# Kernel tuning notes

Measured on AMD Instinct MI355X. Metric: run time of the kernel, lower is better.

The kernel has to match this reference:

```python
import jax, jax.numpy as jnp
import numpy as np

DELAY = 4
SKIP = 2
NF = 8
HS = 256
EPS = 1e-5


def setup_inputs() -> dict:
    key = jax.random.key(0)
    ks = jax.random.split(key, 11)
    B, NP, NO, T = 16, 512, 512, 2048
    predictor = jax.random.normal(ks[0], (B, NP, T), dtype=jnp.float32)
    to_order = jax.random.normal(ks[1], (B, NO, T), dtype=jnp.float32)
    trilinear = jax.random.normal(ks[2], (NF, NO, NP), dtype=jnp.float32) / np.float32(np.sqrt(NP * NO))
    w_o = jax.random.normal(ks[3], (HS, NO), dtype=jnp.float32) / np.float32(np.sqrt(NO))
    b_o = jax.random.normal(ks[4], (HS,), dtype=jnp.float32) * 0.01
    w_p = jax.random.normal(ks[5], (HS, NP), dtype=jnp.float32) / np.float32(np.sqrt(NP))
    b_p = jax.random.normal(ks[6], (HS,), dtype=jnp.float32) * 0.01
    bn_gamma = jnp.ones((HS,), dtype=jnp.float32)
    bn_beta = jnp.zeros((HS,), dtype=jnp.float32)
    w_out = jax.random.normal(ks[7], (NF, HS), dtype=jnp.float32) / np.float32(np.sqrt(HS))
    b_out = jax.random.normal(ks[8], (NF,), dtype=jnp.float32) * 0.01
    return {"predictor": predictor, "to_order": to_order, "trilinear": trilinear,
            "w_o": w_o, "b_o": b_o, "w_p": w_p, "b_p": b_p,
            "bn_gamma": bn_gamma, "bn_beta": bn_beta, "w_out": w_out, "b_out": b_out}


def reference(predictor, to_order, trilinear, w_o, b_o, w_p, b_p, bn_gamma, bn_beta, w_out, b_out):
    B, NP, T = predictor.shape
    NO = to_order.shape[1]
    tot_latency = DELAY + SKIP * (NF - 1)
    T_r = T - tot_latency
    pred = predictor[:, :, :T_r]          # (B, np, Tr)
    too = to_order[:, :, DELAY:]          # (B, no, T - delay)
    # predictor_product[b,k,t,m] = sum_p pred[b,p,t] * trilinear[k,m,p]
    pp = jnp.einsum('bpt,kmp->bktm', pred, trilinear)           # (B, nf, Tr, no)
    win = jnp.stack([too[:, :, j * SKIP: j * SKIP + T_r] for j in range(NF)], axis=1)  # (B, nf, no, Tr)
    inner = jnp.einsum('bjmt,bktm->bjkt', win, pp)              # (B, nf, nf, Tr)
    # conv1d (kernel 1) heads
    o_proj = jnp.einsum('hm,bmt->bht', w_o, too) + b_o[None, :, None]    # (B, hs, T - delay)
    p_proj = jnp.einsum('hp,bpt->bht', w_p, pred) + b_p[None, :, None]   # (B, hs, Tr)
    o_win = jnp.stack([o_proj[:, :, j * SKIP: j * SKIP + T_r] for j in range(NF)], axis=1)  # (B, nf, hs, Tr)
    h = jax.nn.relu(o_win + p_proj[:, None])                    # (B, nf, hs, Tr)
    # BatchNorm1d (training-mode batch stats) over (B*nf, hs, Tr): stats over axes (0,1,3)
    mean = h.mean(axis=(0, 1, 3), keepdims=True)
    var = h.var(axis=(0, 1, 3), keepdims=True)
    h = (h - mean) * jax.lax.rsqrt(var + EPS) * bn_gamma[None, None, :, None] + bn_beta[None, None, :, None]
    head = jnp.einsum('kh,bjht->bjkt', w_out, h) + b_out[None, None, :, None]
    inner = inner + head
    log_probs = jax.nn.log_softmax(inner, axis=2)               # (B, nf, nf, Tr)
    correct = jnp.einsum('bjjt->bjt', log_probs)                # diagonal j == k
    return correct.mean(axis=2).mean(axis=0)                    # (nf,)
```

## Files before the change

kernel.cpp:

```cpp
#include <hip/hip_runtime.h>
#include <math.h>

constexpr int B_  = 16;
constexpr int NP_ = 512;
constexpr int NO_ = 512;
constexpr int T_  = 2048;
constexpr int NF_ = 8;
constexpr int HS_ = 256;
constexpr int TR_ = 2030;
constexpr int TO_ = 2044;
constexpr int OPLD_ = 2048;
constexpr float EPS_ = 1e-5f;

typedef short bf16x8 __attribute__((ext_vector_type(8)));
typedef float f32x16 __attribute__((ext_vector_type(16)));

__device__ __forceinline__ unsigned short f2bf(float f) {
  union { float f; unsigned int u; } v; v.f = f;
  unsigned int r = v.u + 0x7fffu + ((v.u >> 16) & 1u);
  return (unsigned short)(r >> 16);
}
__device__ __forceinline__ float bf2f(unsigned short u) {
  union { unsigned int u; float f; } v; v.u = ((unsigned int)u) << 16;
  return v.f;
}

typedef const __attribute__((address_space(1))) unsigned int* gas_u32;
typedef __attribute__((address_space(3))) unsigned int* las_u32;
__device__ __forceinline__ void gl16(const void* g, void* l) {
  __builtin_amdgcn_global_load_lds((gas_u32)g, (las_u32)l, 16, 0, 0);
}


__global__ __launch_bounds__(256) void transpose_cvt(
    const float* __restrict__ in, unsigned short* __restrict__ outb) {
  __shared__ float tile[64][65];
  const int c0 = blockIdx.x * 64;
  const int r0 = blockIdx.y * 64;
  const int b  = blockIdx.z;
  const float* ib = in + (size_t)b * 512 * 2048;
  unsigned short* ob = outb + (size_t)b * 2048 * 512;
  for (int i = threadIdx.x; i < 64 * 16; i += 256) {
    const int r = i >> 4, c4 = (i & 15) * 4;
    float4 v = *(const float4*)(ib + (size_t)(r0 + r) * 2048 + c0 + c4);
    tile[r][c4 + 0] = v.x; tile[r][c4 + 1] = v.y;
    tile[r][c4 + 2] = v.z; tile[r][c4 + 3] = v.w;
  }
  __syncthreads();
  for (int i = threadIdx.x; i < 64 * 8; i += 256) {
    const int c = i >> 3, r8 = (i & 7) * 8;
    unsigned int pk[4];
    #pragma unroll
    for (int e = 0; e < 4; ++e)
      pk[e] = (unsigned int)f2bf(tile[r8 + 2 * e][c]) |
              ((unsigned int)f2bf(tile[r8 + 2 * e + 1][c]) << 16);
    *(uint4*)(ob + (size_t)(c0 + c) * 512 + r0 + r8) = *(uint4*)pk;
  }
}

__global__ __launch_bounds__(256) void cvt_bf16(
    const float* __restrict__ in, unsigned short* __restrict__ out, int n) {
  const int i = (blockIdx.x * 256 + threadIdx.x) * 4;
  if (i < n) {
    float4 v = *(const float4*)(in + i);
    ushort4 o; o.x = f2bf(v.x); o.y = f2bf(v.y); o.z = f2bf(v.z); o.w = f2bf(v.w);
    *(ushort4*)(out + i) = o;
  }
}

__global__ __launch_bounds__(256, 2) void proj_mfma(
    const unsigned short* __restrict__ Wbf,
    const unsigned short* __restrict__ Xt,
    const float* __restrict__ bias,
    unsigned short* __restrict__ out,
    int Tlen, int toff) {
  __shared__ char smem[65536];
  const int tid = threadIdx.x;
  const int l = tid & 63, wv = tid >> 6;
  const int h = l >> 5, tl = l & 31;
  const int mq = wv >> 1, tq = wv & 1;
  const int t0 = blockIdx.x * 128;
  const int m0 = blockIdx.y * 128;
  const int b  = blockIdx.z;
  const unsigned short* Xb = Xt + (size_t)b * T_ * 512;

  int aSrc[4], bSrc[4], ldsO[4];
  #pragma unroll
  for (int i = 0; i < 4; ++i) {
    const int q = (wv << 8) + (i << 6) + l;
    const int r = q >> 3, c8s = (q & 7) ^ (r & 7);
    aSrc[i] = (m0 + r) * 512 + (c8s << 3);
    const int row = min(t0 + toff + r, T_ - 1);
    bSrc[i] = row * 512 + (c8s << 3);
    ldsO[i] = ((wv << 8) + (i << 6)) << 4;
  }

  f32x16 acc[2][2];
  #pragma unroll
  for (int i = 0; i < 2; ++i)
    #pragma unroll
    for (int jj = 0; jj < 2; ++jj)
      #pragma unroll
      for (int e = 0; e < 16; ++e) acc[i][jj][e] = 0.f;

  #pragma unroll
  for (int i = 0; i < 4; ++i) gl16(Wbf + aSrc[i], smem + ldsO[i]);
  #pragma unroll
  for (int i = 0; i < 4; ++i) gl16(Xb + bSrc[i], smem + 32768 + ldsO[i]);
  asm volatile("s_waitcnt vmcnt(0)" ::: "memory");
  __builtin_amdgcn_s_barrier();

  #pragma unroll
  for (int ps = 0; ps < 8; ++ps) {
    const int cb = ps & 1;
    if (ps < 7) {
      const int p0 = (ps + 1) << 6;
      #pragma unroll
      for (int i = 0; i < 4; ++i)
        gl16(Wbf + p0 + aSrc[i], smem + (cb ^ 1) * 16384 + ldsO[i]);
      #pragma unroll
      for (int i = 0; i < 4; ++i)
        gl16(Xb + p0 + bSrc[i], smem + 32768 + (cb ^ 1) * 16384 + ldsO[i]);
    }
    const unsigned short* As = (const unsigned short*)(smem + cb * 16384);
    const unsigned short* Bs = (const unsigned short*)(smem + 32768 + cb * 16384);
    #pragma unroll
    for (int s = 0; s < 4; ++s) {
      const int k8 = 2 * s + h;
      bf16x8 af[2], bfr[2];
      #pragma unroll
      for (int mt = 0; mt < 2; ++mt) {
        const int rm = 64 * mq + 32 * mt + tl;
        af[mt] = *(const bf16x8*)(As + rm * 64 + ((k8 ^ (rm & 7)) << 3));
      }
      #pragma unroll
      for (int nt = 0; nt < 2; ++nt) {
        const int rt = 64 * tq + 32 * nt + tl;
        bfr[nt] = *(const bf16x8*)(Bs + rt * 64 + ((k8 ^ (rt & 7)) << 3));
      }
      #pragma unroll
      for (int mt = 0; mt < 2; ++mt)
        #pragma unroll
        for (int nt = 0; nt < 2; ++nt)
          acc[mt][nt] = __builtin_amdgcn_mfma_f32_32x32x16_bf16(
              af[mt], bfr[nt], acc[mt][nt], 0, 0, 0);
    }
    asm volatile("s_waitcnt vmcnt(0)" ::: "memory");
    __builtin_amdgcn_s_barrier();
  }
  #pragma unroll
  for (int mt = 0; mt < 2; ++mt)
    #pragma unroll
    for (int nt = 0; nt < 2; ++nt)
      #pragma unroll
      for (int r = 0; r < 16; ++r) {
        const int hs = m0 + 64 * mq + 32 * mt + (r & 3) + 8 * (r >> 2) + 4 * h;
        const int t  = t0 + 64 * tq + 32 * nt + tl;
        if (t < Tlen)
          out[((size_t)b * HS_ + hs) * OPLD_ + t] = f2bf(acc[mt][nt][r] + bias[hs]);
      }
}

__global__ __launch_bounds__(256, 2) void inner_mfma(
    const unsigned short* __restrict__ pred_t,
    const unsigned short* __restrict__ too_t,
    const unsigned short* __restrict__ tri_bf,
    float* __restrict__ inner) {
  __shared__ char smem[81920];
  const int tid = threadIdx.x;
  const int l = tid & 63, wv = tid >> 6;
  const int h = l >> 5, tl = l & 31;
  const int fk = wv & 1, th = wv >> 1;
  const int t0 = blockIdx.x * 128;
  const int kf0 = blockIdx.y * 2;
  const int b  = blockIdx.z;
  const unsigned short* predB = pred_t + (size_t)b * T_ * NP_;
  const unsigned short* tooB  = too_t  + (size_t)b * T_ * NO_;
  const unsigned short* triK  = tri_bf + (size_t)kf0 * NO_ * NP_;

  int pSrc[4], pLds[4];
  #pragma unroll
  for (int i = 0; i < 4; ++i) {
    const int q = (wv << 8) + (i << 6) + l;
    const int r = q >> 3, c8s = (q & 7) ^ (r & 7);
    pSrc[i] = (t0 + r) * NP_ + (c8s << 3);
    pLds[i] = ((wv << 8) + (i << 6)) << 4;
  }
  int tSrc[4], tLds[4];
  #pragma unroll
  for (int i = 0; i < 4; ++i) {
    const int q = (wv << 8) + (i << 6) + l;
    const int f = q >> 9, qq = q & 511;
    const int r = qq >> 3, c8s = (qq & 7) ^ (r & 7);
    tSrc[i] = f * (NO_ * NP_) + r * NP_ + (c8s << 3);
    tLds[i] = ((wv << 8) + (i << 6)) << 4;
  }

  f32x16 Sacc[2][2];
  #pragma unroll
  for (int f = 0; f < 2; ++f)
    #pragma unroll
    for (int ct = 0; ct < 2; ++ct)
      #pragma unroll
      for (int e = 0; e < 16; ++e) Sacc[f][ct][e] = 0.f;

  for (int mc = 0; mc < 8; ++mc) {
    const int m0 = mc << 6;
    const int mOff = m0 * NP_;
    __builtin_amdgcn_s_barrier();
    #pragma unroll
    for (int i = 0; i < 4; ++i) gl16(triK + mOff + tSrc[i], smem + 49152 + tLds[i]);
    #pragma unroll
    for (int i = 0; i < 4; ++i) gl16(predB + pSrc[i], smem + pLds[i]);
    #pragma unroll
    for (int i = 0; i < 4; ++i) gl16(predB + 64 + pSrc[i], smem + 16384 + pLds[i]);

    f32x16 Qacc[2][2];
    #pragma unroll
    for (int mt = 0; mt < 2; ++mt)
      #pragma unroll
      for (int nt = 0; nt < 2; ++nt)
        #pragma unroll
        for (int e = 0; e < 16; ++e) Qacc[mt][nt][e] = 0.f;

    #pragma unroll
    for (int ps = 0; ps < 8; ++ps) {
      const int cb = ps & 1;
      if (ps < 7) asm volatile("s_waitcnt vmcnt(4)" ::: "memory");
      else        asm volatile("s_waitcnt vmcnt(0)" ::: "memory");
      __builtin_amdgcn_s_barrier();
      if (ps < 7) {
        const int p1 = (ps + 1) << 6;
        #pragma unroll
        for (int i = 0; i < 4; ++i)
          gl16(triK + mOff + p1 + tSrc[i],
               smem + 49152 + (cb ^ 1) * 16384 + tLds[i]);
      }
      if (ps < 6) {
        const int p2 = (ps + 2) << 6;
        char* const pb2 = smem + ((ps + 2) % 3) * 16384;
        #pragma unroll
        for (int i = 0; i < 4; ++i)
          gl16(predB + p2 + pSrc[i], pb2 + pLds[i]);
      }
      const unsigned short* predS = (const unsigned short*)(smem + (ps % 3) * 16384);
      const unsigned short* triS  = (const unsigned short*)(smem + 49152 + cb * 16384);
      __builtin_amdgcn_s_setprio(1);
      #pragma unroll
      for (int s = 0; s < 4; ++s) {
        const int k8 = 2 * s + h;
        bf16x8 a[2], bp[2];
        #pragma unroll
        for (int mt = 0; mt < 2; ++mt) {
          const int rm = (mt << 5) + tl;
          a[mt] = *(const bf16x8*)(triS + (fk << 12) + rm * 64 +
                                   ((k8 ^ (rm & 7)) << 3));
        }
        #pragma unroll
        for (int nt = 0; nt < 2; ++nt) {
          const int rb = (th << 6) + (nt << 5) + tl;
          bp[nt] = *(const bf16x8*)(predS + rb * 64 + ((k8 ^ (rb & 7)) << 3));
        }
        #pragma unroll
        for (int mt = 0; mt < 2; ++mt)
          #pragma unroll
          for (int nt = 0; nt < 2; ++nt)
            Qacc[mt][nt] = __builtin_amdgcn_mfma_f32_32x32x16_bf16(
                a[mt], bp[nt], Qacc[mt][nt], 0, 0, 0);
      }
      __builtin_amdgcn_s_setprio(0);
    }
    __builtin_amdgcn_s_barrier();
    #pragma unroll
    for (int nt = 0; nt < 2; ++nt) {
      unsigned short* QSw =
          (unsigned short*)(smem + fk * 16384 + (((th << 1) + nt) << 12));
      #pragma unroll
      for (int mt = 0; mt < 2; ++mt)
        #pragma unroll
        for (int rp = 0; rp < 8; ++rp) {
          const int r = rp << 1;
          const int m = (mt << 5) + (r & 3) + ((r >> 2) << 3) + (h << 2);
          const int c8 = m >> 3, ml = m & 7;
          const int rX = (tl & 24) | ((tl ^ c8) & 7);
          const unsigned int pk = (unsigned int)f2bf(Qacc[mt][nt][r]) |
                                  ((unsigned int)f2bf(Qacc[mt][nt][r + 1]) << 16);
          *(unsigned int*)(QSw + (((c8 << 5) + rX) << 3) + ml) = pk;
        }
    }
    asm volatile("s_waitcnt lgkmcnt(0)" ::: "memory");
    __builtin_amdgcn_s_barrier();
    #pragma unroll
    for (int s = 0; s < 4; ++s) {
      const int k8 = 2 * s + h;
      bf16x8 atoo[2];
      #pragma unroll
      for (int ct = 0; ct < 2; ++ct) {
        const int rr = ((wv + ct) << 5) + tl;
        const int trow = min(t0 + rr, T_ - 1);
        atoo[ct] = *(const bf16x8*)(tooB + (size_t)trow * NO_ + m0 + (k8 << 3));
      }
      const int rqX = (tl & 24) | ((tl ^ k8) & 7);
      #pragma unroll
      for (int f = 0; f < 2; ++f) {
        const bf16x8 bq = *(const bf16x8*)(
            (const unsigned short*)(smem + f * 16384 + (wv << 12)) +
            (((k8 << 5) + rqX) << 3));
        #pragma unroll
        for (int ct = 0; ct < 2; ++ct)
          Sacc[f][ct] = __builtin_amdgcn_mfma_f32_32x32x16_bf16(
              atoo[ct], bq, Sacc[f][ct], 0, 0, 0);
      }
    }
  }
  __syncthreads();
  const int tglob = t0 + (wv << 5) + tl;
  float* SW = (float*)smem + (wv << 11);
  #pragma unroll
  for (int f = 0; f < 2; ++f) {
    #pragma unroll
    for (int ct = 0; ct < 2; ++ct)
      #pragma unroll
      for (int r = 0; r < 16; ++r) {
        const int cc = (ct << 5) + (r & 3) + ((r >> 2) << 3) + (h << 2);
        SW[(cc << 5) + tl] = Sacc[f][ct][r];
      }
    if (tglob < TR_) {
      #pragma unroll
      for (int jj = 0; jj < 4; ++jj) {
        const int j = (jj << 1) + h;
        const float v = SW[((tl + 4 + 2 * j) << 5) + tl];
        inner[(((size_t)b * NF_ + j) * NF_ + (kf0 + f)) * TR_ + tglob] = v;
      }
    }
  }
}

__global__ __launch_bounds__(256) void bn_stats(
    const unsigned short* __restrict__ op, const unsigned short* __restrict__ pp,
    float* __restrict__ partials) {
  const int hh = blockIdx.x, b = blockIdx.y;
  const unsigned short* oprow = op + ((size_t)b * HS_ + hh) * OPLD_;
  const unsigned short* pprow = pp + ((size_t)b * HS_ + hh) * OPLD_;
  float s = 0.f, s2 = 0.f;
  for (int t = threadIdx.x; t < TR_; t += 256) {
    const float pv = bf2f(pprow[t]);
    #pragma unroll
    for (int j = 0; j < NF_; ++j) {
      float r = bf2f(oprow[t + 2 * j]) + pv;
      r = fmaxf(r, 0.f);
      s += r; s2 += r * r;
    }
  }
  __shared__ float red[256], red2[256];
  red[threadIdx.x] = s; red2[threadIdx.x] = s2;
  __syncthreads();
  for (int st = 128; st > 0; st >>= 1) {
    if (threadIdx.x < st) {
      red[threadIdx.x]  += red[threadIdx.x + st];
      red2[threadIdx.x] += red2[threadIdx.x + st];
    }
    __syncthreads();
  }
  if (threadIdx.x == 0) {
    partials[b * HS_ + hh]            = red[0];
    partials[B_ * HS_ + b * HS_ + hh] = red2[0];
  }
}

__global__ __launch_bounds__(256) void bn_finalize(
    const float* __restrict__ partials, const float* __restrict__ gamma,
    const float* __restrict__ beta, const float* __restrict__ w_out,
    const float* __restrict__ b_out, float* __restrict__ w_eff,
    float* __restrict__ cvec) {
  const int hh = threadIdx.x;
  float s = 0.f, s2 = 0.f;
  for (int b = 0; b < B_; ++b) {
    s  += partials[b * HS_ + hh];
    s2 += partials[B_ * HS_ + b * HS_ + hh];
  }
  const float cnt  = (float)B_ * NF_ * TR_;
  const float mean = s / cnt;
  const float var  = s2 / cnt - mean * mean;
  const float scale = gamma[hh] * rsqrtf(var + EPS_);
  const float shift = beta[hh] - mean * scale;
  #pragma unroll
  for (int k = 0; k < NF_; ++k) w_eff[k * HS_ + hh] = w_out[k * HS_ + hh] * scale;
  __shared__ float red[256];
  for (int k = 0; k < NF_; ++k) {
    red[hh] = w_out[k * HS_ + hh] * shift;
    __syncthreads();
    for (int st = 128; st > 0; st >>= 1) {
      if (hh < st) red[hh] += red[hh + st];
      __syncthreads();
    }
    if (hh == 0) cvec[k] = b_out[k] + red[0];
    __syncthreads();
  }
}

__global__ __launch_bounds__(256) void head_final(
    const unsigned short* __restrict__ op, const unsigned short* __restrict__ pp,
    const float* __restrict__ w_eff, const float* __restrict__ cvec,
    const float* __restrict__ inner, float* __restrict__ part3) {
  __shared__ float opS[288 * 20];
  __shared__ float ppS[256 * 20];
  __shared__ float weS[8][256];
  __shared__ float red[4][5];
  const int tid = threadIdx.x;
  const int t0 = blockIdx.x * 256;
  const int b  = blockIdx.y;
  const int jh = blockIdx.z;
  for (int i = tid; i < 8 * 256; i += 256) weS[i >> 8][i & 255] = w_eff[i];
  float acc[4][8] = {};
  const unsigned short* opb = op + (size_t)b * HS_ * OPLD_;
  const unsigned short* ppb = pp + (size_t)b * HS_ * OPLD_;
  for (int hc = 0; hc < 16; ++hc) {
    const int h0 = hc << 4;
    __syncthreads();
    for (int idx = tid; idx < 576; idx += 256) {
      const int r = idx / 36, cc = (idx - r * 36) << 3;
      const int g = min(t0 + cc, OPLD_ - 8);
      uint4 v = *(const uint4*)(opb + (size_t)(h0 + r) * OPLD_ + g);
      #pragma unroll
      for (int e = 0; e < 4; ++e) {
        const unsigned int u = (&v.x)[e];
        opS[(cc + 2 * e) * 20 + r]     = bf2f((unsigned short)(u & 0xffffu));
        opS[(cc + 2 * e + 1) * 20 + r] = bf2f((unsigned short)(u >> 16));
      }
    }
    for (int idx = tid; idx < 512; idx += 256) {
      const int r = idx >> 5, cc = (idx & 31) << 3;
      uint4 v = *(const uint4*)(ppb + (size_t)(h0 + r) * OPLD_ + t0 + cc);
      #pragma unroll
      for (int e = 0; e < 4; ++e) {
        const unsigned int u = (&v.x)[e];
        ppS[(cc + 2 * e) * 20 + r]     = bf2f((unsigned short)(u & 0xffffu));
        ppS[(cc + 2 * e + 1) * 20 + r] = bf2f((unsigned short)(u >> 16));
      }
    }
    __syncthreads();
    float pv[16];
    #pragma unroll
    for (int i = 0; i < 4; ++i) {
      float4 q = *(const float4*)(ppS + tid * 20 + 4 * i);
      pv[4 * i + 0] = q.x; pv[4 * i + 1] = q.y;
      pv[4 * i + 2] = q.z; pv[4 * i + 3] = q.w;
    }
    #pragma unroll
    for (int jj = 0; jj < 4; ++jj) {
      const int col = tid + 2 * ((jh << 2) + jj);
      #pragma unroll
      for (int i = 0; i < 4; ++i) {
        float4 ov = *(const float4*)(opS + col * 20 + 4 * i);
        #pragma unroll
        for (int e = 0; e < 4; ++e) {
          const float r = fmaxf((&ov.x)[e] + pv[4 * i + e], 0.f);
          #pragma unroll
          for (int k = 0; k < 8; ++k) acc[jj][k] += weS[k][h0 + 4 * i + e] * r;
        }
      }
    }
  }
  const int t = t0 + tid;
  float sj[4];
  #pragma unroll
  for (int jj = 0; jj < 4; ++jj) {
    if (t < TR_) {
      const int j = (jh << 2) + jj;
      float v[8]; float mx = -1e30f;
      #pragma unroll
      for (int k = 0; k < 8; ++k) {
        v[k] = acc[jj][k] + cvec[k] +
               inner[(((size_t)b * NF_ + j) * NF_ + k) * TR_ + t];
        mx = fmaxf(mx, v[k]);
      }
      float se = 0.f;
      #pragma unroll
      for (int k = 0; k < 8; ++k) se += expf(v[k] - mx);
      sj[jj] = v[j] - mx - logf(se);
    } else sj[jj] = 0.f;
  }
  #pragma unroll
  for (int jj = 0; jj < 4; ++jj)
    #pragma unroll
    for (int off = 32; off > 0; off >>= 1) sj[jj] += __shfl_down(sj[jj], off);
  if ((tid & 63) == 0) {
    const int wv = tid >> 6;
    #pragma unroll
    for (int jj = 0; jj < 4; ++jj) red[jj][wv] = sj[jj];
  }
  __syncthreads();
  if (tid < 4) {
    const float s = red[tid][0] + red[tid][1] + red[tid][2] + red[tid][3];
    const int j = (jh << 2) + tid;
    part3[(j * B_ + b) * 8 + blockIdx.x] = s;
  }
}

__global__ void final_out(const float* __restrict__ part3, float* __restrict__ out) {
  const int j = threadIdx.x;
  if (j < NF_) {
    float s = 0.f;
    for (int i = 0; i < B_ * 8; ++i) s += part3[j * B_ * 8 + i];
    out[j] = s / ((float)B_ * (float)TR_);
  }
}

extern "C" void kernel_launch(void* const* d_in, const int* in_sizes, int n_in,
                              void* d_out, int out_size, void* d_ws, size_t ws_size,
                              hipStream_t stream) {
  const float* predictor = (const float*)d_in[0];
  const float* to_order  = (const float*)d_in[1];
  const float* trilinear = (const float*)d_in[2];
  const float* w_o   = (const float*)d_in[3];
  const float* b_o   = (const float*)d_in[4];
  const float* w_p   = (const float*)d_in[5];
  const float* b_p   = (const float*)d_in[6];
  const float* bn_g  = (const float*)d_in[7];
  const float* bn_b  = (const float*)d_in[8];
  const float* w_out = (const float*)d_in[9];
  const float* b_out = (const float*)d_in[10];
  float* out = (float*)d_out;

  char* w = (char*)d_ws;
  unsigned short* pred_t = (unsigned short*)w; w += (size_t)B_ * T_ * NP_ * 2;
  unsigned short* too_t  = (unsigned short*)w; w += (size_t)B_ * T_ * NO_ * 2;
  unsigned short* tri_bf = (unsigned short*)w; w += (size_t)NF_ * NO_ * NP_ * 2;
  unsigned short* wo_bf  = (unsigned short*)w; w += (size_t)HS_ * NO_ * 2;
  unsigned short* wp_bf  = (unsigned short*)w; w += (size_t)HS_ * NP_ * 2;
  unsigned short* o_proj = (unsigned short*)w; w += (size_t)B_ * HS_ * OPLD_ * 2;
  unsigned short* p_proj = (unsigned short*)w; w += (size_t)B_ * HS_ * OPLD_ * 2;
  float* inner    = (float*)w; w += (size_t)B_ * NF_ * NF_ * TR_ * 4;
  float* partials = (float*)w; w += (size_t)2 * B_ * HS_ * 4;
  float* w_eff    = (float*)w; w += (size_t)NF_ * HS_ * 4;
  float* cvec     = (float*)w; w += 256;
  float* part3    = (float*)w; w += (size_t)NF_ * B_ * 8 * 4;

  transpose_cvt<<<dim3(32, 8, 16), 256, 0, stream>>>(predictor, pred_t);
  transpose_cvt<<<dim3(32, 8, 16), 256, 0, stream>>>(to_order, too_t);
  cvt_bf16<<<2048, 256, 0, stream>>>(trilinear, tri_bf, NF_ * NO_ * NP_);
  cvt_bf16<<<128, 256, 0, stream>>>(w_o, wo_bf, HS_ * NO_);
  cvt_bf16<<<128, 256, 0, stream>>>(w_p, wp_bf, HS_ * NP_);

  proj_mfma<<<dim3(16, 2, 16), 256, 0, stream>>>(wo_bf, too_t, b_o, o_proj, TO_, 4);
  proj_mfma<<<dim3(16, 2, 16), 256, 0, stream>>>(wp_bf, pred_t, b_p, p_proj, TR_, 0);

  inner_mfma<<<dim3(16, 4, 16), 256, 0, stream>>>(pred_t, too_t, tri_bf, inner);

  bn_stats<<<dim3(HS_, B_), 256, 0, stream>>>(o_proj, p_proj, partials);
  bn_finalize<<<1, 256, 0, stream>>>(partials, bn_g, bn_b, w_out, b_out, w_eff, cvec);
  head_final<<<dim3(8, B_, 2), 256, 0, stream>>>(o_proj, p_proj, w_eff, cvec, inner, part3);
  final_out<<<1, 64, 0, stream>>>(part3, out);
}
```

Measured before the change: 371.3 us.

## Stage to_order tiles in LDS and switch pred to double buffering

The second GEMM stage used to read to_order straight from global memory. It now loads those tiles into shared memory through async global-to-LDS copies: part of the tile is fetched at the start of each m-chunk, and the rest goes into the freed trilinear buffer after the last p-step. To free the space, pred goes from triple buffering to double buffering, and each p-step now waits for vmcnt(0) and hits a barrier at its end. This cuts scattered global loads in the inner product but reduces prefetch depth, which exposes more memory latency in the first GEMM loop.

```diff
diff --git a/kernel.cpp b/kernel.cpp
--- a/kernel.cpp
+++ b/kernel.cpp
@@ -166,7 +166,7 @@
     const unsigned short* __restrict__ too_t,
     const unsigned short* __restrict__ tri_bf,
     float* __restrict__ inner) {
-  __shared__ char smem[81920];
+  __shared__ char smem[77824];
   const int tid = threadIdx.x;
   const int l = tid & 63, wv = tid >> 6;
   const int h = l >> 5, tl = l & 31;
@@ -195,6 +195,22 @@
     tSrc[i] = f * (NO_ * NP_) + r * NP_ + (c8s << 3);
     tLds[i] = ((wv << 8) + (i << 6)) << 4;
   }
+  int oSrc[3], oLds[3];
+  #pragma unroll
+  for (int i = 0; i < 3; ++i) {
+    const int q = wv * 192 + (i << 6) + l;
+    const int r = q >> 3, c8s = (q & 7) ^ (r & 7);
+    oSrc[i] = (t0 + r) * NO_ + (c8s << 3);
+    oLds[i] = (wv * 192 + (i << 6)) << 4;
+  }
+  int aSrcT[2], aLdsT[2];
+  #pragma unroll
+  for (int i = 0; i < 2; ++i) {
+    const int q = (wv << 7) + (i << 6) + l;
+    const int r = 96 + (q >> 3), c8s = (q & 7) ^ (r & 7);
+    aSrcT[i] = min(t0 + r, T_ - 1) * NO_ + (c8s << 3);
+    aLdsT[i] = q << 4;
+  }
 
   f32x16 Sacc[2][2];
   #pragma unroll
@@ -209,11 +225,13 @@
     const int mOff = m0 * NP_;
     __builtin_amdgcn_s_barrier();
     #pragma unroll
-    for (int i = 0; i < 4; ++i) gl16(triK + mOff + tSrc[i], smem + 49152 + tLds[i]);
+    for (int i = 0; i < 3; ++i) gl16(tooB + m0 + oSrc[i], smem + 65536 + oLds[i]);
+    #pragma unroll
+    for (int i = 0; i < 4; ++i) gl16(triK + mOff + tSrc[i], smem + 32768 + tLds[i]);
     #pragma unroll
     for (int i = 0; i < 4; ++i) gl16(predB + pSrc[i], smem + pLds[i]);
-    #pragma unroll
-    for (int i = 0; i < 4; ++i) gl16(predB + 64 + pSrc[i], smem + 16384 + pLds[i]);
+    asm volatile("s_waitcnt vmcnt(0)" ::: "memory");
+    __builtin_amdgcn_s_barrier();
 
     f32x16 Qacc[2][2];
     #pragma unroll
@@ -226,25 +244,18 @@
     #pragma unroll
     for (int ps = 0; ps < 8; ++ps) {
       const int cb = ps & 1;
-      if (ps < 7) asm volatile("s_waitcnt vmcnt(4)" ::: "memory");
-      else        asm volatile("s_waitcnt vmcnt(0)" ::: "memory");
-      __builtin_amdgcn_s_barrier();
       if (ps < 7) {
         const int p1 = (ps + 1) << 6;
         #pragma unroll
         for (int i = 0; i < 4; ++i)
           gl16(triK + mOff + p1 + tSrc[i],
-               smem + 49152 + (cb ^ 1) * 16384 + tLds[i]);
-      }
-      if (ps < 6) {
-        const int p2 = (ps + 2) << 6;
-        char* const pb2 = smem + ((ps + 2) % 3) * 16384;
+               smem + 32768 + (cb ^ 1) * 16384 + tLds[i]);
         #pragma unroll
         for (int i = 0; i < 4; ++i)
-          gl16(predB + p2 + pSrc[i], pb2 + pLds[i]);
-      }
-      const unsigned short* predS = (const unsigned short*)(smem + (ps % 3) * 16384);
-      const unsigned short* triS  = (const unsigned short*)(smem + 49152 + cb * 16384);
+          gl16(predB + p1 + pSrc[i], smem + (cb ^ 1) * 16384 + pLds[i]);
+      }
+      const unsigned short* predS = (const unsigned short*)(smem + cb * 16384);
+      const unsigned short* triS  = (const unsigned short*)(smem + 32768 + cb * 16384);
       __builtin_amdgcn_s_setprio(1);
       #pragma unroll
       for (int s = 0; s < 4; ++s) {
@@ -269,8 +280,14 @@
                 a[mt], bp[nt], Qacc[mt][nt], 0, 0, 0);
       }
       __builtin_amdgcn_s_setprio(0);
-    }
-    __builtin_amdgcn_s_barrier();
+      if (ps == 7) {
+        #pragma unroll
+        for (int i = 0; i < 2; ++i)
+          gl16(tooB + m0 + aSrcT[i], smem + 32768 + aLdsT[i]);
+      }
+      asm volatile("s_waitcnt vmcnt(0)" ::: "memory");
+      __builtin_amdgcn_s_barrier();
+    }
     #pragma unroll
     for (int nt = 0; nt < 2; ++nt) {
       unsigned short* QSw =
@@ -297,8 +314,10 @@
       #pragma unroll
       for (int ct = 0; ct < 2; ++ct) {
         const int rr = ((wv + ct) << 5) + tl;
-        const int trow = min(t0 + rr, T_ - 1);
-        atoo[ct] = *(const bf16x8*)(tooB + (size_t)trow * NO_ + m0 + (k8 << 3));
+        const unsigned short* tb = (rr < 96)
+            ? (const unsigned short*)(smem + 65536) + (size_t)rr * 64
+            : (const unsigned short*)(smem + 32768) + (size_t)(rr - 96) * 64;
+        atoo[ct] = *(const bf16x8*)(tb + ((k8 ^ (rr & 7)) << 3));
       }
       const int rqX = (tl & 24) | ((tl ^ k8) & 7);
       #pragma unroll
```

Measured after the change: 387.1 us. 1.04x slower.
